# Kernel tuning notes

Measured on AMD Instinct MI355X. Metric: run time of the kernel, lower is better.

## Reference

```python
import jax, jax.numpy as jnp
import numpy as np

DIM = 1024
NUM_HEADS = 16
HEAD_DIM = DIM // NUM_HEADS
SCALE = HEAD_DIM ** (-0.5)


def setup_inputs() -> dict:
    key = jax.random.key(0)
    ks = jax.random.split(key, 5)
    B, L, D = 2, 2048, DIM
    x = jax.random.normal(ks[0], (B, L, D), dtype=jnp.float32)
    # torch nn.Linear init scale ~ U(-1/sqrt(fan_in), 1/sqrt(fan_in)); use small normals
    s = 1.0 / np.sqrt(D)
    qkv_w = jax.random.uniform(ks[1], (3 * D, D), minval=-s, maxval=s, dtype=jnp.float32)
    qkv_b = jax.random.uniform(ks[2], (3 * D,), minval=-s, maxval=s, dtype=jnp.float32)
    proj_w = jax.random.uniform(ks[3], (D, D), minval=-s, maxval=s, dtype=jnp.float32)
    proj_b = jax.random.uniform(ks[4], (D,), minval=-s, maxval=s, dtype=jnp.float32)
    return {"x": x, "qkv_w": qkv_w, "qkv_b": qkv_b, "proj_w": proj_w, "proj_b": proj_b}


def reference(x, qkv_w, qkv_b, proj_w, proj_b):
    B, L, D = x.shape
    H, Hd = NUM_HEADS, HEAD_DIM
    # QKV projection: [B,L,3D] -> [3,B,H,L,Hd]
    qkv = x @ qkv_w.T + qkv_b
    qkv = qkv.reshape(B, L, 3, H, Hd).transpose(2, 0, 3, 1, 4)
    q, k, v = qkv[0], qkv[1], qkv[2]
    scores = jnp.einsum('bhqd,bhkd->bhqk', q, k) * SCALE  # [B,H,L,L]
    attn = jax.nn.softmax(scores, axis=-1)
    out = jnp.einsum('bhqk,bhkd->bhqd', attn, v)  # [B,H,L,Hd]
    out = out.transpose(0, 2, 1, 3).reshape(B, L, D)
    out = out @ proj_w.T + proj_b
    return out
```

## Files before the change

### kernel.cpp

```cpp
#include <hip/hip_runtime.h>
#include <hip/hip_bf16.h>
#include <cstdint>
#include <cstddef>

#define D_MODEL 1024
#define NHEADS 16
#define HD 64
#define NB 2
#define SL 2048
#define SEQ (NB*SL)
#define NQKV (3*D_MODEL)

typedef __attribute__((ext_vector_type(8))) short short8;
typedef __attribute__((ext_vector_type(4))) float floatx4;
typedef __attribute__((ext_vector_type(16))) float f32x16;
typedef unsigned short u16;

__device__ __forceinline__ u16 f2bf(float f) {
    union { float f; uint32_t u; } v; v.f = f;
    return (u16)((v.u + 0x7fffu + ((v.u >> 16) & 1u)) >> 16);
}

__device__ __forceinline__ uint32_t cvt_pk_bf16(float lo, float hi) {
    uint32_t r;
    asm("v_cvt_pk_bf16_f32 %0, %1, %2" : "=v"(r) : "v"(lo), "v"(hi));
    return r;
}

__device__ __forceinline__ void pl32swap(uint32_t &a, uint32_t &b) {
    asm("v_permlane32_swap_b32 %0, %1" : "+v"(a), "+v"(b));
}

__device__ __forceinline__ f32x16 zero16() {
    f32x16 z;
    #pragma unroll
    for (int i = 0; i < 16; i++) z[i] = 0.f;
    return z;
}

#define GLDS(gsrc, ldst) __builtin_amdgcn_global_load_lds( \
    (const __attribute__((address_space(1))) void*)(gsrc), \
    (__attribute__((address_space(3))) void*)(ldst), 16, 0, 0)

__global__ __launch_bounds__(256) void cvt_kernel(const float* __restrict__ in,
                                                  u16* __restrict__ out, int n4) {
    int i = blockIdx.x * 256 + threadIdx.x;
    if (i >= n4) return;
    float4 f = ((const float4*)in)[i];
    ushort4 o;
    o.x = f2bf(f.x); o.y = f2bf(f.y); o.z = f2bf(f.z); o.w = f2bf(f.w);
    ((ushort4*)out)[i] = o;
}

__device__ __forceinline__ void gemm128_staged(const u16* __restrict__ A,
                                               const u16* __restrict__ B,
                                               int mbase, int nbase, int K,
                                               u16* Alds, u16* Blds,
                                               floatx4 acc[4][4]) {
    const int tid = threadIdx.x;
    const int lane = tid & 63;
    const int l15 = lane & 15, quad = lane >> 4;
    const int wave = tid >> 6;
    const int wr = wave >> 1, wc = wave & 1;
    #pragma unroll
    for (int i = 0; i < 4; i++)
        #pragma unroll
        for (int j = 0; j < 4; j++)
            acc[i][j] = (floatx4){0.f, 0.f, 0.f, 0.f};

    const int r0 = tid >> 2, kg0 = (tid & 3) * 8;
    const int r1 = (256 + tid) >> 2, kg1 = kg0;
    const u16* Arow0 = A + (size_t)(mbase + r0) * K + kg0;
    const u16* Arow1 = A + (size_t)(mbase + r1) * K + kg1;
    const u16* Brow0 = B + (size_t)(nbase + r0) * K + kg0;
    const u16* Brow1 = B + (size_t)(nbase + r1) * K + kg1;

    for (int k0 = 0; k0 < K; k0 += 32) {
        __syncthreads();
        GLDS(Arow0 + k0, Alds + tid * 8);
        GLDS(Arow1 + k0, Alds + (256 + tid) * 8);
        GLDS(Brow0 + k0, Blds + tid * 8);
        GLDS(Brow1 + k0, Blds + (256 + tid) * 8);
        __syncthreads();

        short8 af[4], bf[4];
        #pragma unroll
        for (int i = 0; i < 4; i++)
            af[i] = *(const short8*)(Alds + (wr * 64 + i * 16 + l15) * 32 + quad * 8);
        #pragma unroll
        for (int j = 0; j < 4; j++)
            bf[j] = *(const short8*)(Blds + (wc * 64 + j * 16 + l15) * 32 + quad * 8);
        #pragma unroll
        for (int i = 0; i < 4; i++)
            #pragma unroll
            for (int j = 0; j < 4; j++)
                acc[i][j] = __builtin_amdgcn_mfma_f32_16x16x32_bf16(af[i], bf[j], acc[i][j], 0, 0, 0);
    }
}

__global__ __launch_bounds__(256) void qkv_gemm(const u16* __restrict__ xb,
                                                const u16* __restrict__ wb,
                                                const float* __restrict__ bias,
                                                u16* __restrict__ Qo, u16* __restrict__ Ko,
                                                u16* __restrict__ Vt) {
    __shared__ __align__(16) u16 Alds[128 * 32];
    __shared__ __align__(16) u16 Blds[128 * 32];
    const int mbase = blockIdx.y * 128;
    const int nbase = blockIdx.x * 128;
    floatx4 acc[4][4];
    gemm128_staged(xb, wb, mbase, nbase, 1024, Alds, Blds, acc);
    const int lane = threadIdx.x & 63;
    const int wave = threadIdx.x >> 6;
    const int wr = wave >> 1, wc = wave & 1;
    const int l15 = lane & 15, quad = lane >> 4;
    #pragma unroll
    for (int j = 0; j < 4; j++) {
        int n = nbase + wc * 64 + j * 16 + l15;
        float bv = bias[n];
        int which = n >> 10;
        int within = n & 1023;
        int h = within >> 6, d = within & 63;
        #pragma unroll
        for (int i = 0; i < 4; i++) {
            #pragma unroll
            for (int r = 0; r < 4; r++) {
                int m = mbase + wr * 64 + i * 16 + quad * 4 + r;
                int b = m >> 11, l = m & 2047;
                int bh = b * NHEADS + h;
                float v = acc[i][j][r] + bv;
                if (which == 0) {
                    Qo[((size_t)bh * SL + l) * HD + d] = f2bf(v * 0.125f);
                } else if (which == 1) {
                    int slot = ((l >> 5) & 1) * 256 + (d >> 4) * 64 + ((d >> 3) & 1) * 32 + (l & 31);
                    Ko[(size_t)bh * (SL * HD) + (size_t)(l >> 6) * 4096 + slot * 8 + (d & 7)] = f2bf(v);
                } else {
                    int slot = ((l >> 5) & 1) * 256 + ((l >> 4) & 1) * 128 + (d >> 5) * 64 + ((l >> 3) & 1) * 32 + (d & 31);
                    Vt[(size_t)bh * (SL * HD) + (size_t)(l >> 6) * 4096 + slot * 8 + (l & 7)] = f2bf(v);
                }
            }
        }
    }
}

__global__ __launch_bounds__(256, 2) void flash_kernel(const u16* __restrict__ Q,
                                                       const u16* __restrict__ K,
                                                       const u16* __restrict__ V,
                                                       u16* __restrict__ AO) {
    __shared__ __align__(16) u16 Klds[2 * 4096];
    __shared__ __align__(16) u16 Vlds[2 * 4096];
    const int tid = threadIdx.x;
    const int lane = tid & 63;
    const int wave = tid >> 6;
    const int hi = lane >> 5;
    const int l31 = lane & 31;
    const int lane8 = lane * 8;

    const int bid = (int)blockIdx.x;
    const int swz = (bid & 7) * 64 + (bid >> 3);
    const int bh = swz >> 4;
    const int qb = swz & 15;
    const int b = bh >> 4, h = bh & 15;
    const int qbase = qb * 128 + wave * 32;

    const u16* Qp = Q + (size_t)bh * SL * HD;
    const u16* Kg = K + (size_t)bh * (SL * HD);
    const u16* Vg = V + (size_t)bh * (SL * HD);

    short8 qf[4];
    #pragma unroll
    for (int c = 0; c < 4; c++)
        qf[c] = *(const short8*)(Qp + (size_t)(qbase + l31) * HD + c * 16 + hi * 8);

    f32x16 accO0 = zero16(), accO1 = zero16();
    float m_i = -__builtin_inff();
    float l_i = 0.f;

    GLDS(Kg + tid * 8,         Klds + tid * 8);
    GLDS(Kg + (256 + tid) * 8, Klds + (256 + tid) * 8);
    GLDS(Vg + tid * 8,         Vlds + tid * 8);
    GLDS(Vg + (256 + tid) * 8, Vlds + (256 + tid) * 8);
    __syncthreads();

    union PW { uint32_t w[4]; short8 s8; };

    for (int t = 0; t < SL / 64; t++) {
        const int cur = t & 1;
        if (t + 1 < SL / 64) {
            const u16* ks = Kg + (size_t)(t + 1) * 4096;
            const u16* vs = Vg + (size_t)(t + 1) * 4096;
            u16* kd = Klds + (cur ^ 1) * 4096;
            u16* vd = Vlds + (cur ^ 1) * 4096;
            GLDS(ks + tid * 8,         kd + tid * 8);
            GLDS(ks + (256 + tid) * 8, kd + (256 + tid) * 8);
            GLDS(vs + tid * 8,         vd + tid * 8);
            GLDS(vs + (256 + tid) * 8, vd + (256 + tid) * 8);
        }
        const u16* Kt  = Klds + cur * 4096;
        const u16* Vt_ = Vlds + cur * 4096;

        f32x16 sA = zero16(), sB = zero16();
        #pragma unroll
        for (int c = 0; c < 4; c++) {
            short8 kf = *(const short8*)(Kt + c * 512 + lane8);
            sA = __builtin_amdgcn_mfma_f32_32x32x16_bf16(kf, qf[c], sA, 0, 0, 0);
        }
        #pragma unroll
        for (int c = 0; c < 4; c++) {
            short8 kf = *(const short8*)(Kt + 2048 + c * 512 + lane8);
            sB = __builtin_amdgcn_mfma_f32_32x32x16_bf16(kf, qf[c], sB, 0, 0, 0);
        }

        float mx = fmaxf(sA[0], sA[1]);
        #pragma unroll
        for (int e = 2; e < 16; e++) mx = fmaxf(mx, sA[e]);
        #pragma unroll
        for (int e = 0; e < 16; e++) mx = fmaxf(mx, sB[e]);
        mx = fmaxf(mx, __shfl_xor(mx, 32, 64));
        const float mnew = fmaxf(m_i, mx);
        const float alpha = __expf(m_i - mnew);
        m_i = mnew;
        float rs = 0.f;
        #pragma unroll
        for (int e = 0; e < 16; e++) { float p = __expf(sA[e] - mnew); sA[e] = p; rs += p; }
        #pragma unroll
        for (int e = 0; e < 16; e++) { float p = __expf(sB[e] - mnew); sB[e] = p; rs += p; }
        rs += __shfl_xor(rs, 32, 64);
        l_i = l_i * alpha + rs;
        #pragma unroll
        for (int e = 0; e < 16; e++) { accO0[e] *= alpha; accO1[e] *= alpha; }

#define PV_SUB(SV, OFF) { \
        uint32_t a0 = cvt_pk_bf16(SV[0], SV[1]);  uint32_t b0 = cvt_pk_bf16(SV[4], SV[5]);  pl32swap(a0, b0); \
        uint32_t a1 = cvt_pk_bf16(SV[2], SV[3]);  uint32_t b1 = cvt_pk_bf16(SV[6], SV[7]);  pl32swap(a1, b1); \
        PW f0; f0.w[0] = a0; f0.w[1] = a1; f0.w[2] = b0; f0.w[3] = b1; \
        accO0 = __builtin_amdgcn_mfma_f32_32x32x16_bf16(*(const short8*)(Vt_ + (OFF) + lane8),        f0.s8, accO0, 0, 0, 0); \
        accO1 = __builtin_amdgcn_mfma_f32_32x32x16_bf16(*(const short8*)(Vt_ + (OFF) + 512 + lane8),  f0.s8, accO1, 0, 0, 0); \
        uint32_t c0 = cvt_pk_bf16(SV[8], SV[9]);  uint32_t d0 = cvt_pk_bf16(SV[12], SV[13]); pl32swap(c0, d0); \
        uint32_t c1 = cvt_pk_bf16(SV[10], SV[11]); uint32_t d1 = cvt_pk_bf16(SV[14], SV[15]); pl32swap(c1, d1); \
        PW f1; f1.w[0] = c0; f1.w[1] = c1; f1.w[2] = d0; f1.w[3] = d1; \
        accO0 = __builtin_amdgcn_mfma_f32_32x32x16_bf16(*(const short8*)(Vt_ + (OFF) + 1024 + lane8),       f1.s8, accO0, 0, 0, 0); \
        accO1 = __builtin_amdgcn_mfma_f32_32x32x16_bf16(*(const short8*)(Vt_ + (OFF) + 1024 + 512 + lane8), f1.s8, accO1, 0, 0, 0); }

        PV_SUB(sA, 0);
        PV_SUB(sB, 2048);
#undef PV_SUB

        __syncthreads();
    }

    const float invl = 1.f / l_i;
    const int qrow = qbase + l31;
    const size_t rowbase = ((size_t)(b * SL + qrow)) * D_MODEL + h * HD;
    #pragma unroll
    for (int rg = 0; rg < 4; rg++) {
        ushort4 o0, o1;
        o0.x = f2bf(accO0[rg * 4 + 0] * invl); o0.y = f2bf(accO0[rg * 4 + 1] * invl);
        o0.z = f2bf(accO0[rg * 4 + 2] * invl); o0.w = f2bf(accO0[rg * 4 + 3] * invl);
        *(ushort4*)(AO + rowbase + rg * 8 + 4 * hi) = o0;
        o1.x = f2bf(accO1[rg * 4 + 0] * invl); o1.y = f2bf(accO1[rg * 4 + 1] * invl);
        o1.z = f2bf(accO1[rg * 4 + 2] * invl); o1.w = f2bf(accO1[rg * 4 + 3] * invl);
        *(ushort4*)(AO + rowbase + 32 + rg * 8 + 4 * hi) = o1;
    }
}

__global__ __launch_bounds__(256) void proj_gemm(const u16* __restrict__ ab,
                                                 const u16* __restrict__ wb,
                                                 const float* __restrict__ bias,
                                                 float* __restrict__ out) {
    __shared__ __align__(16) u16 Alds[128 * 32];
    __shared__ __align__(16) u16 Blds[128 * 32];
    const int mbase = blockIdx.y * 128;
    const int nbase = blockIdx.x * 128;
    floatx4 acc[4][4];
    gemm128_staged(ab, wb, mbase, nbase, 1024, Alds, Blds, acc);
    const int lane = threadIdx.x & 63;
    const int wave = threadIdx.x >> 6;
    const int wr = wave >> 1, wc = wave & 1;
    const int l15 = lane & 15, quad = lane >> 4;
    #pragma unroll
    for (int j = 0; j < 4; j++) {
        int n = nbase + wc * 64 + j * 16 + l15;
        float bv = bias[n];
        #pragma unroll
        for (int i = 0; i < 4; i++) {
            #pragma unroll
            for (int r = 0; r < 4; r++) {
                int m = mbase + wr * 64 + i * 16 + quad * 4 + r;
                out[(size_t)m * D_MODEL + n] = acc[i][j][r] + bv;
            }
        }
    }
}

extern "C" void kernel_launch(void* const* d_in, const int* in_sizes, int n_in,
                              void* d_out, int out_size, void* d_ws, size_t ws_size,
                              hipStream_t stream) {
    const float* x      = (const float*)d_in[0];
    const float* qkv_w  = (const float*)d_in[1];
    const float* qkv_b  = (const float*)d_in[2];
    const float* proj_w = (const float*)d_in[3];
    const float* proj_b = (const float*)d_in[4];
    float* out = (float*)d_out;
    char* ws = (char*)d_ws;

    u16* xb    = (u16*)(ws);
    u16* wqkv  = (u16*)(ws + 8388608);
    u16* wproj = (u16*)(ws + 14680064);
    u16* Qb    = (u16*)(ws + 16777216);
    u16* Kb    = (u16*)(ws + 25165824);
    u16* Vt    = (u16*)(ws + 33554432);
    u16* AO    = (u16*)(ws + 41943040);

    cvt_kernel<<<4096, 256, 0, stream>>>(x, xb, 4194304 / 4);
    cvt_kernel<<<3072, 256, 0, stream>>>(qkv_w, wqkv, 3145728 / 4);
    cvt_kernel<<<1024, 256, 0, stream>>>(proj_w, wproj, 1048576 / 4);
    qkv_gemm<<<dim3(NQKV / 128, SEQ / 128), 256, 0, stream>>>(xb, wqkv, qkv_b, Qb, Kb, Vt);
    flash_kernel<<<dim3(512), 256, 0, stream>>>(Qb, Kb, Vt, AO);
    proj_gemm<<<dim3(D_MODEL / 128, SEQ / 128), 256, 0, stream>>>(AO, wproj, proj_b, out);
}
```

Before: 219.7 us.

## Use exp2 softmax with lazy rescaling, MFMA priority hints, and fused conversion launch

Folds log2(e) into the Q scaling so the flash kernel can use raw v_exp_f32, and skips the max update and accumulator rescale unless some lane's new max exceeds the running max by more than 24. It also restructures the max and sum reductions into a tree form, raises wave priority around the MFMA blocks, and merges three fp32-to-bf16 conversion launches into one. The goal is to cut transcendental and VALU cost in the softmax and launch overhead. Lazy rescaling relies on the fp32 exponent range when probabilities exceed one before normalization.

```diff
diff --git a/kernel.cpp b/kernel.cpp
--- a/kernel.cpp
+++ b/kernel.cpp
@@ -31,6 +31,23 @@
     asm("v_permlane32_swap_b32 %0, %1" : "+v"(a), "+v"(b));
 }
 
+__device__ __forceinline__ float exp2f_fast(float x) {
+    float r; asm("v_exp_f32 %0, %1" : "=v"(r) : "v"(x)); return r;
+}
+
+__device__ __forceinline__ float m3f(float a, float b, float c) {
+    return fmaxf(fmaxf(a, b), c);
+}
+
+__device__ __forceinline__ float vmax16(const f32x16& v) {
+    float a0 = m3f(v[0], v[1], v[2]);
+    float a1 = m3f(v[3], v[4], v[5]);
+    float a2 = m3f(v[6], v[7], v[8]);
+    float a3 = m3f(v[9], v[10], v[11]);
+    float a4 = m3f(v[12], v[13], v[14]);
+    return fmaxf(m3f(a0, a1, v[15]), m3f(a2, a3, a4));
+}
+
 __device__ __forceinline__ f32x16 zero16() {
     f32x16 z;
     #pragma unroll
@@ -42,14 +59,21 @@
     (const __attribute__((address_space(1))) void*)(gsrc), \
     (__attribute__((address_space(3))) void*)(ldst), 16, 0, 0)
 
-__global__ __launch_bounds__(256) void cvt_kernel(const float* __restrict__ in,
-                                                  u16* __restrict__ out, int n4) {
+__global__ __launch_bounds__(256) void cvt_all(const float* __restrict__ x,
+                                               const float* __restrict__ w1,
+                                               const float* __restrict__ w2,
+                                               u16* __restrict__ xb,
+                                               u16* __restrict__ w1b,
+                                               u16* __restrict__ w2b) {
     int i = blockIdx.x * 256 + threadIdx.x;
-    if (i >= n4) return;
-    float4 f = ((const float4*)in)[i];
+    const float4* src; ushort4* dst; int j;
+    if (i < 1048576)      { src = (const float4*)x;  dst = (ushort4*)xb;  j = i; }
+    else if (i < 1835008) { src = (const float4*)w1; dst = (ushort4*)w1b; j = i - 1048576; }
+    else                  { src = (const float4*)w2; dst = (ushort4*)w2b; j = i - 1835008; }
+    float4 f = src[j];
     ushort4 o;
     o.x = f2bf(f.x); o.y = f2bf(f.y); o.z = f2bf(f.z); o.w = f2bf(f.w);
-    ((ushort4*)out)[i] = o;
+    dst[j] = o;
 }
 
 __device__ __forceinline__ void gemm128_staged(const u16* __restrict__ A,
@@ -129,7 +153,7 @@
                 int bh = b * NHEADS + h;
                 float v = acc[i][j][r] + bv;
                 if (which == 0) {
-                    Qo[((size_t)bh * SL + l) * HD + d] = f2bf(v * 0.125f);
+                    Qo[((size_t)bh * SL + l) * HD + d] = f2bf(v * 0.18033688f);
                 } else if (which == 1) {
                     int slot = ((l >> 5) & 1) * 256 + (d >> 4) * 64 + ((d >> 3) & 1) * 32 + (l & 31);
                     Ko[(size_t)bh * (SL * HD) + (size_t)(l >> 6) * 4096 + slot * 8 + (d & 7)] = f2bf(v);
@@ -199,6 +223,7 @@
         const u16* Vt_ = Vlds + cur * 4096;
 
         f32x16 sA = zero16(), sB = zero16();
+        __builtin_amdgcn_s_setprio(1);
         #pragma unroll
         for (int c = 0; c < 4; c++) {
             short8 kf = *(const short8*)(Kt + c * 512 + lane8);
@@ -209,25 +234,34 @@
             short8 kf = *(const short8*)(Kt + 2048 + c * 512 + lane8);
             sB = __builtin_amdgcn_mfma_f32_32x32x16_bf16(kf, qf[c], sB, 0, 0, 0);
         }
-
-        float mx = fmaxf(sA[0], sA[1]);
-        #pragma unroll
-        for (int e = 2; e < 16; e++) mx = fmaxf(mx, sA[e]);
-        #pragma unroll
-        for (int e = 0; e < 16; e++) mx = fmaxf(mx, sB[e]);
-        mx = fmaxf(mx, __shfl_xor(mx, 32, 64));
-        const float mnew = fmaxf(m_i, mx);
-        const float alpha = __expf(m_i - mnew);
-        m_i = mnew;
-        float rs = 0.f;
-        #pragma unroll
-        for (int e = 0; e < 16; e++) { float p = __expf(sA[e] - mnew); sA[e] = p; rs += p; }
-        #pragma unroll
-        for (int e = 0; e < 16; e++) { float p = __expf(sB[e] - mnew); sB[e] = p; rs += p; }
+        __builtin_amdgcn_s_setprio(0);
+
+        float pmax = fmaxf(vmax16(sA), vmax16(sB));
+        if (!__all(pmax - m_i <= 24.0f)) {
+            float mo = m_i;
+            float mn = fmaxf(mo, fmaxf(pmax, __shfl_xor(pmax, 32, 64)));
+            m_i = mn;
+            float alpha = exp2f_fast(mo - mn);
+            l_i *= alpha;
+            #pragma unroll
+            for (int e = 0; e < 16; e++) { accO0[e] *= alpha; accO1[e] *= alpha; }
+        }
+        #pragma unroll
+        for (int e = 0; e < 16; e++) sA[e] = exp2f_fast(sA[e] - m_i);
+        #pragma unroll
+        for (int e = 0; e < 16; e++) sB[e] = exp2f_fast(sB[e] - m_i);
+        float r0 = 0.f, r1 = 0.f, r2 = 0.f, r3 = 0.f;
+        #pragma unroll
+        for (int e = 0; e < 16; e += 4) {
+            r0 += sA[e]; r1 += sA[e + 1]; r2 += sA[e + 2]; r3 += sA[e + 3];
+        }
+        #pragma unroll
+        for (int e = 0; e < 16; e += 4) {
+            r0 += sB[e]; r1 += sB[e + 1]; r2 += sB[e + 2]; r3 += sB[e + 3];
+        }
+        float rs = (r0 + r1) + (r2 + r3);
         rs += __shfl_xor(rs, 32, 64);
-        l_i = l_i * alpha + rs;
-        #pragma unroll
-        for (int e = 0; e < 16; e++) { accO0[e] *= alpha; accO1[e] *= alpha; }
+        l_i += rs;
 
 #define PV_SUB(SV, OFF) { \
         uint32_t a0 = cvt_pk_bf16(SV[0], SV[1]);  uint32_t b0 = cvt_pk_bf16(SV[4], SV[5]);  pl32swap(a0, b0); \
@@ -241,8 +275,10 @@
         accO0 = __builtin_amdgcn_mfma_f32_32x32x16_bf16(*(const short8*)(Vt_ + (OFF) + 1024 + lane8),       f1.s8, accO0, 0, 0, 0); \
         accO1 = __builtin_amdgcn_mfma_f32_32x32x16_bf16(*(const short8*)(Vt_ + (OFF) + 1024 + 512 + lane8), f1.s8, accO1, 0, 0, 0); }
 
+        __builtin_amdgcn_s_setprio(1);
         PV_SUB(sA, 0);
         PV_SUB(sB, 2048);
+        __builtin_amdgcn_s_setprio(0);
 #undef PV_SUB
 
         __syncthreads();
@@ -311,9 +347,7 @@
     u16* Vt    = (u16*)(ws + 33554432);
     u16* AO    = (u16*)(ws + 41943040);
 
-    cvt_kernel<<<4096, 256, 0, stream>>>(x, xb, 4194304 / 4);
-    cvt_kernel<<<3072, 256, 0, stream>>>(qkv_w, wqkv, 3145728 / 4);
-    cvt_kernel<<<1024, 256, 0, stream>>>(proj_w, wproj, 1048576 / 4);
+    cvt_all<<<8192, 256, 0, stream>>>(x, qkv_w, proj_w, xb, wqkv, wproj);
     qkv_gemm<<<dim3(NQKV / 128, SEQ / 128), 256, 0, stream>>>(xb, wqkv, qkv_b, Qb, Kb, Vt);
     flash_kernel<<<dim3(512), 256, 0, stream>>>(Qb, Kb, Vt, AO);
     proj_gemm<<<dim3(D_MODEL / 128, SEQ / 128), 256, 0, stream>>>(AO, wproj, proj_b, out);
```

After: 207.3 us. 1.06x faster.
